# Optimization experiments

Hardware: AMD Instinct MI355X
Metric: run time of the kernel (lower is better)

## Reference

```python
import jax, jax.numpy as jnp
from jax import lax
import numpy as np

N, T, PD, TD, F, E, GB = 2048, 256, 5, 5, 128, 65536, 5


def _lstm_layer(x, Wih, Whh, bih, bhh):
    # x: [B, T, D] -> [B, T, H], torch LSTM gate order (i, f, g, o)
    B = x.shape[0]
    H = Whh.shape[1]
    b = bih + bhh

    def step(carry, xt):
        h, c = carry
        gates = xt @ Wih.T + h @ Whh.T + b
        i, f, g, o = jnp.split(gates, 4, axis=-1)
        c = jax.nn.sigmoid(f) * c + jax.nn.sigmoid(i) * jnp.tanh(g)
        h = jax.nn.sigmoid(o) * jnp.tanh(c)
        return (h, c), h

    h0 = jnp.zeros((B, H), x.dtype)
    _, hs = lax.scan(step, (h0, h0), jnp.swapaxes(x, 0, 1))
    return jnp.swapaxes(hs, 0, 1)


def _attention(x, W1, b1, W2, b2):
    # Fused prefix (cumulative causal) softmax attention.
    # Original loops over t computing softmax(scores[:, :t+1]); here:
    # ctx[t] = cumsum(e * x)[t] / cumsum(e)[t] with a global max shift
    # (softmax is shift-invariant, so this equals the per-prefix softmax).
    s = (jnp.tanh(x @ W1.T + b1) @ W2.T + b2)[..., 0]  # [B, T]
    e = jnp.exp(s - jnp.max(s, axis=1, keepdims=True))  # [B, T]
    num = jnp.cumsum(e[..., None] * x, axis=1)          # [B, T, D]
    den = jnp.cumsum(e, axis=1)[..., None]              # [B, T, 1]
    return jnp.sum(num / den, axis=1)                   # [B, D]


def _gcn(x, W, b, edge_index, edge_weight):
    # PyG GCNConv with normalize=True: add self-loops (w=1), symmetric norm.
    n = x.shape[0]
    loop = jnp.arange(n)
    row = jnp.concatenate([edge_index[0], loop])
    col = jnp.concatenate([edge_index[1], loop])
    w = jnp.concatenate([edge_weight, jnp.ones((n,), edge_weight.dtype)])
    deg = jax.ops.segment_sum(w, col, num_segments=n)
    dinv = jnp.where(deg > 0, deg ** -0.5, 0.0)
    norm = dinv[row] * w * dinv[col]
    h = x @ W.T
    out = jax.ops.segment_sum(norm[:, None] * h[row], col, num_segments=n)
    return out + b


def _forward(price, global_trend, p_weights, t_weights,
             lp_Wih0, lp_Whh0, lp_bih0, lp_bhh0, lp_Wih1, lp_Whh1, lp_bih1, lp_bhh1,
             lt_Wih0, lt_Whh0, lt_bih0, lt_bhh0, lt_Wih1, lt_Whh1, lt_bih1, lt_bhh1,
             ap_W1, ap_b1, ap_W2, ap_b2, at_W1, at_b1, at_W2, at_b2,
             gp1_W, gp1_b, gp2_W, gp2_b, gt1_W, gt1_b, gt2_W, gt2_b,
             mlp_W, mlp_b, p_edge_index, t_edge_index):
    x = _lstm_layer(price, lp_Wih0, lp_Whh0, lp_bih0, lp_bhh0)
    x = _lstm_layer(x, lp_Wih1, lp_Whh1, lp_bih1, lp_bhh1)
    x = _attention(x, ap_W1, ap_b1, ap_W2, ap_b2)            # [N, F]
    g = _lstm_layer(global_trend, lt_Wih0, lt_Whh0, lt_bih0, lt_bhh0)
    g = _lstm_layer(g, lt_Wih1, lt_Whh1, lt_bih1, lt_bhh1)
    g = _attention(g, at_W1, at_b1, at_W2, at_b2)            # [GB, F]
    pg = _gcn(x, gp1_W, gp1_b, p_edge_index, p_weights)
    pg = _gcn(pg, gp2_W, gp2_b, p_edge_index, p_weights)     # [N, F]
    # NOTE: original feeds x (not g) into the trend graph convs.
    tg = _gcn(x, gt1_W, gt1_b, t_edge_index, t_weights)
    tg = _gcn(tg, gt2_W, gt2_b, t_edge_index, t_weights)     # [N, F]
    trend = tg @ g.T                                         # [N, GB]
    feat = jnp.concatenate([pg, trend], axis=1)              # [N, F+GB]
    return jax.nn.sigmoid(feat @ mlp_W.T + mlp_b)            # [N, 1]


def setup_inputs() -> dict:
    key = jax.random.key(0)
    ks = iter(jax.random.split(key, 64))
    nrm = lambda shape, s=0.05: jax.random.normal(next(ks), shape, jnp.float32) * s
    inp = {}
    inp['price'] = jax.random.normal(next(ks), (N, T, PD), jnp.float32)
    inp['global_trend'] = jax.random.normal(next(ks), (GB, T, TD), jnp.float32)
    inp['p_edge_index'] = jax.random.randint(next(ks), (2, E), 0, N)
    inp['p_weights'] = jax.random.uniform(next(ks), (E,), jnp.float32)
    inp['t_edge_index'] = jax.random.randint(next(ks), (2, E), 0, N)
    inp['t_weights'] = jax.random.uniform(next(ks), (E,), jnp.float32)
    for pre, d in (('lp', PD), ('lt', TD)):
        inp[pre + '_Wih0'] = nrm((4 * F, d)); inp[pre + '_Whh0'] = nrm((4 * F, F))
        inp[pre + '_bih0'] = nrm((4 * F,));   inp[pre + '_bhh0'] = nrm((4 * F,))
        inp[pre + '_Wih1'] = nrm((4 * F, F)); inp[pre + '_Whh1'] = nrm((4 * F, F))
        inp[pre + '_bih1'] = nrm((4 * F,));   inp[pre + '_bhh1'] = nrm((4 * F,))
    for pre in ('ap', 'at'):
        inp[pre + '_W1'] = nrm((F, F)); inp[pre + '_b1'] = jnp.zeros((F,), jnp.float32)
        inp[pre + '_W2'] = nrm((1, F)); inp[pre + '_b2'] = jnp.zeros((1,), jnp.float32)
    for pre in ('gp', 'gt'):
        inp[pre + '1_W'] = nrm((16, F)); inp[pre + '1_b'] = jnp.zeros((16,), jnp.float32)
        inp[pre + '2_W'] = nrm((F, 16)); inp[pre + '2_b'] = jnp.zeros((F,), jnp.float32)
    inp['mlp_W'] = nrm((1, F + GB)); inp['mlp_b'] = jnp.zeros((1,), jnp.float32)
    return inp


def reference(price, global_trend, p_edge_index, p_weights, t_edge_index, t_weights,
              lp_Wih0, lp_Whh0, lp_bih0, lp_bhh0, lp_Wih1, lp_Whh1, lp_bih1, lp_bhh1,
              lt_Wih0, lt_Whh0, lt_bih0, lt_bhh0, lt_Wih1, lt_Whh1, lt_bih1, lt_bhh1,
              ap_W1, ap_b1, ap_W2, ap_b2, at_W1, at_b1, at_W2, at_b2,
              gp1_W, gp1_b, gp2_W, gp2_b, gt1_W, gt1_b, gt2_W, gt2_b,
              mlp_W, mlp_b):
    return _forward(price, global_trend, p_weights, t_weights,
                    lp_Wih0, lp_Whh0, lp_bih0, lp_bhh0, lp_Wih1, lp_Whh1, lp_bih1, lp_bhh1,
                    lt_Wih0, lt_Whh0, lt_bih0, lt_bhh0, lt_Wih1, lt_Whh1, lt_bih1, lt_bhh1,
                    ap_W1, ap_b1, ap_W2, ap_b2, at_W1, at_b1, at_W2, at_b2,
                    gp1_W, gp1_b, gp2_W, gp2_b, gt1_W, gt1_b, gt2_W, gt2_b,
                    mlp_W, mlp_b, p_edge_index, t_edge_index)
```

## Files before the change

kernel.cpp:

```cpp
#include <hip/hip_runtime.h>
#include <hip/hip_bf16.h>
#include <cstddef>

#define TT    256
#define NROW  2048
#define GBN   5
#define EDG   65536

using f32x4  = __attribute__((ext_vector_type(4))) float;
using bf16x8 = __attribute__((ext_vector_type(8))) short;

__device__ __forceinline__ void pinv(bf16x8& x) { asm volatile("" : "+v"(x)); }

__device__ __forceinline__ void barrier_lgkm() {
  asm volatile("s_waitcnt lgkmcnt(0)" ::: "memory");
  __builtin_amdgcn_s_barrier();
}

enum : int {
  PK_P0  = 0,
  PK_P1  = 65536,
  PK_PA  = 196608,
  PK_T0  = 212992,
  PK_T1  = 278528,
  PK_TA  = 409600,
  XBUF   = 425984,
  GBUFO  = 688128,
  DINVP  = 688768,
  DINVT  = 690816,
  H16    = 692864,
  PG1    = 725632,
  H128   = 758400,
  PGB    = 1020544,
  TG1    = 1282688,
  TGB    = 1315456,
  WS_END = 1577600
};

enum : int {
  N_P0   = 0,
  N_P1I  = 65536,
  N_P1H  = 131072,
  N_PA   = 196608,
  N_T0   = 212992,
  N_T1I  = 278528,
  N_T1H  = 344064,
  N_TA   = 409600
};

enum : long long {
  C0S_O   = 1577600,
  C1S_O   = 1841792,
  H1IMG_O = 2105984,
  SMST_O  = 2370176,
  NUMS_O  = 2374304,
  ACCOS_O = 2638496,
  H0S_O   = 2902688
};

__device__ __forceinline__ float sigf(float x) { return 1.0f / (1.0f + __expf(-x)); }
__device__ __forceinline__ float tanh_fast(float x) { return 2.0f * sigf(2.0f * x) - 1.0f; }

__global__ void k_pack(const float* __restrict__ Wa, const float* __restrict__ Wb,
                       int K1, int K2, int NT, int KS, ushort* __restrict__ dst) {
  int t = blockIdx.x * blockDim.x + threadIdx.x;
  int total = KS * NT * 2 * 64;
  if (t >= total) return;
  int lane = t & 63;
  int part = (t >> 6) & 1;
  int rest = t >> 7;
  int nt = rest % NT, kk = rest / NT;
  int j = nt * 16 + (lane & 15);
  int kbase = kk * 32 + (lane >> 4) * 8;
  bf16x8 o;
  #pragma unroll
  for (int e = 0; e < 8; ++e) {
    int k = kbase + e;
    float x = (k < K1) ? Wa[(size_t)j * K1 + k] : Wb[(size_t)j * K2 + (k - K1)];
    __hip_bfloat16 hi = __float2bfloat16(x);
    ushort u;
    if (part == 0) {
      u = *(ushort*)&hi;
    } else {
      float lo = x - __bfloat162float(hi);
      __hip_bfloat16 lob = __float2bfloat16(lo);
      u = *(ushort*)&lob;
    }
    o[e] = (short)u;
  }
  ((bf16x8*)dst)[t] = o;
}

__global__ void k_zero(float* __restrict__ p, int n) {
  int i = blockIdx.x * blockDim.x + threadIdx.x;
  if (i < n) p[i] = 0.0f;
}
__global__ void k_fill1(float* __restrict__ p, int n) {
  int i = blockIdx.x * blockDim.x + threadIdx.x;
  if (i < n) p[i] = 1.0f;
}
__global__ void k_deg(const int* __restrict__ col, const float* __restrict__ w,
                      float* __restrict__ deg, int n) {
  int i = blockIdx.x * blockDim.x + threadIdx.x;
  if (i < n) atomicAdd(&deg[col[i]], w[i]);
}
__global__ void k_dinv(float* __restrict__ deg, int n) {
  int i = blockIdx.x * blockDim.x + threadIdx.x;
  if (i < n) deg[i] = rsqrtf(deg[i]);
}

__global__ __launch_bounds__(512, 2) void k_lstm0(
    const float* __restrict__ price, const float* __restrict__ gtrend,
    const float* __restrict__ ws_ro, ushort* __restrict__ h0S, float* __restrict__ c0S,
    const float* __restrict__ Wih0p, const float* __restrict__ bi0p, const float* __restrict__ bh0p,
    const float* __restrict__ Wih0t, const float* __restrict__ bi0t, const float* __restrict__ bh0t,
    int nPrice, int t0, int TCp, int first)
{
  const int tid = threadIdx.x;
  const int w = tid >> 6, l = tid & 63;
  const int lq = l >> 4, lr = l & 15;
  const int rb = lq * 4;
  const int kcol = w * 16 + lr;
  const bool isP = ((int)blockIdx.x) < nPrice;
  const int R = isP ? 16 : GBN;
  const float* seq = isP ? (price + (size_t)blockIdx.x * 16 * (TT * 5)) : gtrend;
  const ushort* S0 = (const ushort*)(ws_ro + (isP ? N_P0 : N_T0));
  const float* Wih0 = isP ? Wih0p : Wih0t;
  const float* bi0 = isP ? bi0p : bi0t;
  const float* bh0 = isP ? bh0p : bh0t;

  __shared__ __align__(16) ushort h0hi[2048], h0lo[2048];
  __shared__ float xs[2][16][5];

  bf16x8 wh[4][4], wl[4][4];
  #pragma unroll
  for (int kk = 0; kk < 4; ++kk)
    #pragma unroll
    for (int g = 0; g < 4; ++g) {
      int blk = (kk * 32 + (w + 8 * g)) * 2;
      wh[kk][g] = ((const bf16x8*)S0)[(blk + 0) * 64 + l];
      wl[kk][g] = ((const bf16x8*)S0)[(blk + 1) * 64 + l];
      pinv(wh[kk][g]); pinv(wl[kk][g]);
    }
  float wih0r[4][5], bg0[4];
  #pragma unroll
  for (int g = 0; g < 4; ++g) {
    int j = kcol + 128 * g;
    bg0[g] = bi0[j] + bh0[j];
    #pragma unroll
    for (int k = 0; k < 5; ++k) wih0r[g][k] = Wih0[j * 5 + k];
  }

  const size_t bstr = (size_t)blockIdx.x * (size_t)TCp * 4096;
  float c0[4] = {0, 0, 0, 0};

  if (first) {
    for (int i = tid; i < 2048; i += 512) { h0hi[i] = 0; h0lo[i] = 0; }
  } else {
    const size_t lb = bstr + (size_t)(TCp - 1) * 4096;
    *(uint2*)&h0hi[4 * tid] = *(const uint2*)&h0S[lb + 4 * tid];
    *(uint2*)&h0lo[4 * tid] = *(const uint2*)&h0S[lb + 2048 + 4 * tid];
    #pragma unroll
    for (int reg = 0; reg < 4; ++reg)
      c0[reg] = c0S[(size_t)blockIdx.x * 2048 + (size_t)(rb + reg) * 128 + kcol];
  }
  const bool stager = (tid >= 64 && tid < 144);
  const int sr = stager ? (tid - 64) / 5 : 0;
  const int sk = stager ? (tid - 64) % 5 : 0;
  if (stager) {
    xs[0][sr][sk] = (sr < R) ? seq[(size_t)sr * (TT * 5) + t0 * 5 + sk] : 0.0f;
  }
  __syncthreads();

  const int kkhi = (kcol >> 3) & 3;
  const int eo = kcol & 7;
  const int b0w = rb + 16 * kkhi;
  const int kkw = kcol >> 5;
  int wro[4];
  #pragma unroll
  for (int reg = 0; reg < 4; ++reg) wro[reg] = kkw * 512 + (b0w + (reg ^ lq)) * 8 + eo;
  const int rdo = (l ^ ((l >> 2) & 3)) * 8;

  for (int tl = 0; tl < TCp; ++tl) {
    const int xb = tl & 1;
    float xld = 0.0f;
    if (stager && tl + 1 < TCp)
      xld = (sr < R) ? seq[(size_t)sr * (TT * 5) + (size_t)(t0 + tl + 1) * 5 + sk] : 0.0f;

    f32x4 acc[4];
    #pragma unroll
    for (int g = 0; g < 4; ++g) acc[g] = (f32x4){bg0[g], bg0[g], bg0[g], bg0[g]};
    #pragma unroll
    for (int k = 0; k < 5; ++k) {
      float xv[4];
      #pragma unroll
      for (int reg = 0; reg < 4; ++reg) xv[reg] = xs[xb][rb + reg][k];
      #pragma unroll
      for (int g = 0; g < 4; ++g)
        #pragma unroll
        for (int reg = 0; reg < 4; ++reg)
          acc[g][reg] = fmaf(xv[reg], wih0r[g][k], acc[g][reg]);
    }
    #pragma unroll
    for (int kk = 0; kk < 4; ++kk) {
      bf16x8 ah = *(const bf16x8*)&h0hi[kk * 512 + rdo];
      bf16x8 al = *(const bf16x8*)&h0lo[kk * 512 + rdo];
      #pragma unroll
      for (int g = 0; g < 4; ++g) {
        acc[g] = __builtin_amdgcn_mfma_f32_16x16x32_bf16(ah, wh[kk][g], acc[g], 0, 0, 0);
        acc[g] = __builtin_amdgcn_mfma_f32_16x16x32_bf16(al, wh[kk][g], acc[g], 0, 0, 0);
        acc[g] = __builtin_amdgcn_mfma_f32_16x16x32_bf16(ah, wl[kk][g], acc[g], 0, 0, 0);
      }
    }
    barrier_lgkm();
    #pragma unroll
    for (int reg = 0; reg < 4; ++reg) {
      float gi = acc[0][reg], gf = acc[1][reg], gg = acc[2][reg], go = acc[3][reg];
      float c = sigf(gf) * c0[reg] + sigf(gi) * tanh_fast(gg);
      c0[reg] = c;
      float h = sigf(go) * tanh_fast(c);
      __hip_bfloat16 hb = __float2bfloat16(h);
      float lo = h - __bfloat162float(hb);
      __hip_bfloat16 lb = __float2bfloat16(lo);
      h0hi[wro[reg]] = *(ushort*)&hb;
      h0lo[wro[reg]] = *(ushort*)&lb;
    }
    if (stager && tl + 1 < TCp) xs[xb ^ 1][sr][sk] = xld;
    barrier_lgkm();
    *(uint2*)&h0S[bstr + (size_t)tl * 4096 + 4 * tid] = *(const uint2*)&h0hi[4 * tid];
    *(uint2*)&h0S[bstr + (size_t)tl * 4096 + 2048 + 4 * tid] = *(const uint2*)&h0lo[4 * tid];
  }

  #pragma unroll
  for (int reg = 0; reg < 4; ++reg)
    c0S[(size_t)blockIdx.x * 2048 + (size_t)(rb + reg) * 128 + kcol] = c0[reg];
}

__global__ __launch_bounds__(512, 2) void k_pre1(
    const ushort* __restrict__ h0S, const float* __restrict__ ws_ro,
    float* __restrict__ pre1,
    const float* __restrict__ bi1p, const float* __restrict__ bh1p,
    const float* __restrict__ bi1t, const float* __restrict__ bh1t,
    int nPrice, int TCp, int nsub)
{
  const int b = blockIdx.x / nsub, sub = blockIdx.x % nsub;
  const int tid = threadIdx.x;
  const int w = tid >> 6, l = tid & 63;
  const int lr = l & 15;
  const int kcol = w * 16 + lr;
  const bool isP = b < nPrice;
  const ushort* S1I = (const ushort*)(ws_ro + (isP ? N_P1I : N_T1I));
  const float* bi1 = isP ? bi1p : bi1t;
  const float* bh1 = isP ? bh1p : bh1t;
  float bg1[4];
  #pragma unroll
  for (int g = 0; g < 4; ++g) bg1[g] = bi1[kcol + 128 * g] + bh1[kcol + 128 * g];
  const int rdo = (l ^ ((l >> 2) & 3)) * 8;
  const size_t bstr = (size_t)b * (size_t)TCp * 4096;
  const int t0 = sub * 4;

  f32x4 acc[4][4];
  #pragma unroll
  for (int ts = 0; ts < 4; ++ts)
    #pragma unroll
    for (int g = 0; g < 4; ++g) acc[ts][g] = (f32x4){bg1[g], bg1[g], bg1[g], bg1[g]};

  #pragma unroll
  for (int kk = 0; kk < 4; ++kk) {
    bf16x8 bh_[4], bl_[4];
    #pragma unroll
    for (int g = 0; g < 4; ++g) {
      int blk = (kk * 32 + (w + 8 * g)) * 2;
      bh_[g] = ((const bf16x8*)S1I)[(blk + 0) * 64 + l];
      bl_[g] = ((const bf16x8*)S1I)[(blk + 1) * 64 + l];
    }
    #pragma unroll
    for (int ts = 0; ts < 4; ++ts) {
      const size_t tb = bstr + (size_t)(t0 + ts) * 4096 + kk * 512 + rdo;
      bf16x8 ah = *(const bf16x8*)&h0S[tb];
      bf16x8 al = *(const bf16x8*)&h0S[tb + 2048];
      #pragma unroll
      for (int g = 0; g < 4; ++g) {
        acc[ts][g] = __builtin_amdgcn_mfma_f32_16x16x32_bf16(ah, bh_[g], acc[ts][g], 0, 0, 0);
        acc[ts][g] = __builtin_amdgcn_mfma_f32_16x16x32_bf16(al, bh_[g], acc[ts][g], 0, 0, 0);
        acc[ts][g] = __builtin_amdgcn_mfma_f32_16x16x32_bf16(ah, bl_[g], acc[ts][g], 0, 0, 0);
      }
    }
  }
  #pragma unroll
  for (int ts = 0; ts < 4; ++ts)
    #pragma unroll
    for (int g = 0; g < 4; ++g)
      *(f32x4*)&pre1[((size_t)b * TCp + (t0 + ts)) * 8192 + (size_t)tid * 16 + g * 4] = acc[ts][g];
}

__global__ __launch_bounds__(512, 2) void k_lstm1(
    const float* __restrict__ pre1, const float* __restrict__ ws_ro,
    float* __restrict__ xout, float* __restrict__ gout,
    float* __restrict__ c1S, ushort* __restrict__ h1imgS, float* __restrict__ smS,
    float* __restrict__ numS, float* __restrict__ accOS,
    const float* __restrict__ apB1, const float* __restrict__ apW2, const float* __restrict__ apB2,
    const float* __restrict__ atB1, const float* __restrict__ atW2, const float* __restrict__ atB2,
    int nPrice, int t0, int TCp, int first)
{
  const int tid = threadIdx.x;
  const int w = tid >> 6, l = tid & 63;
  const int lq = l >> 4, lr = l & 15;
  const int rb = lq * 4;
  const int kcol = w * 16 + lr;
  const bool isP = ((int)blockIdx.x) < nPrice;
  const int R = isP ? 16 : GBN;
  const ushort* S1H = (const ushort*)(ws_ro + (isP ? N_P1H : N_T1H));
  const ushort* SA  = (const ushort*)(ws_ro + (isP ? N_PA : N_TA));
  const float* b1ap = isP ? apB1 : atB1;
  const float* w2p  = isP ? apW2 : atW2;
  const float  b2v  = isP ? apB2[0] : atB2[0];

  __shared__ __align__(16) ushort h1hi[2048], h1lo[2048];
  __shared__ float sbuf[8][16];

  bf16x8 hh[4][4], hl[4][4];
  #pragma unroll
  for (int kk = 0; kk < 4; ++kk)
    #pragma unroll
    for (int g = 0; g < 4; ++g) {
      int blk = (kk * 32 + (w + 8 * g)) * 2;
      hh[kk][g] = ((const bf16x8*)S1H)[(blk + 0) * 64 + l];
      hl[kk][g] = ((const bf16x8*)S1H)[(blk + 1) * 64 + l];
      pinv(hh[kk][g]); pinv(hl[kk][g]);
    }
  bf16x8 wa[4], wal[4];
  #pragma unroll
  for (int kk = 0; kk < 4; ++kk) {
    wa[kk]  = ((const bf16x8*)SA)[((kk * 8 + w) * 2 + 0) * 64 + l];
    wal[kk] = ((const bf16x8*)SA)[((kk * 8 + w) * 2 + 1) * 64 + l];
    pinv(wa[kk]); pinv(wal[kk]);
  }
  const float w2r = w2p[kcol], b1ar = b1ap[kcol];

  float c1[4] = {0, 0, 0, 0}, h1r[4] = {0, 0, 0, 0};
  float num[4] = {0, 0, 0, 0}, accO[4] = {0, 0, 0, 0};
  float m_run[4], den_r[4];

  if (first) {
    for (int i = tid; i < 2048; i += 512) { h1hi[i] = 0; h1lo[i] = 0; }
    #pragma unroll
    for (int reg = 0; reg < 4; ++reg) { m_run[reg] = -1e30f; den_r[reg] = 0.0f; }
  } else {
    const size_t ib = (size_t)blockIdx.x * 4096;
    *(uint2*)&h1hi[4 * tid] = *(const uint2*)&h1imgS[ib + 4 * tid];
    *(uint2*)&h1lo[4 * tid] = *(const uint2*)&h1imgS[ib + 2048 + 4 * tid];
    const size_t sb = (size_t)blockIdx.x * 2048;
    #pragma unroll
    for (int reg = 0; reg < 4; ++reg) {
      size_t o = sb + (size_t)(rb + reg) * 128 + kcol;
      c1[reg] = c1S[o];
      num[reg] = numS[o];
      accO[reg] = accOS[o];
      m_run[reg] = smS[(size_t)blockIdx.x * 32 + (size_t)(rb + reg) * 2];
      den_r[reg] = smS[(size_t)blockIdx.x * 32 + (size_t)(rb + reg) * 2 + 1];
    }
  }
  __syncthreads();

  const int kkhi = (kcol >> 3) & 3;
  const int eo = kcol & 7;
  const int b0w = rb + 16 * kkhi;
  const int kkw = kcol >> 5;
  int wro[4];
  #pragma unroll
  for (int reg = 0; reg < 4; ++reg) wro[reg] = kkw * 512 + (b0w + (reg ^ lq)) * 8 + eo;
  const int rdo = (l ^ ((l >> 2) & 3)) * 8;

  const float* pbase = pre1 + (size_t)blockIdx.x * TCp * 8192 + (size_t)tid * 16;

  f32x4 pnext[4];
  #pragma unroll
  for (int g = 0; g < 4; ++g) pnext[g] = *(const f32x4*)&pbase[g * 4];

  for (int tl = 0; tl < TCp; ++tl) {
    f32x4 acc[4];
    #pragma unroll
    for (int g = 0; g < 4; ++g) acc[g] = pnext[g];
    if (tl + 1 < TCp) {
      #pragma unroll
      for (int g = 0; g < 4; ++g)
        pnext[g] = *(const f32x4*)&pbase[(size_t)(tl + 1) * 8192 + g * 4];
    }

    #pragma unroll
    for (int kk = 0; kk < 4; ++kk) {
      bf16x8 ah = *(const bf16x8*)&h1hi[kk * 512 + rdo];
      bf16x8 al = *(const bf16x8*)&h1lo[kk * 512 + rdo];
      #pragma unroll
      for (int g = 0; g < 4; ++g) {
        acc[g] = __builtin_amdgcn_mfma_f32_16x16x32_bf16(ah, hh[kk][g], acc[g], 0, 0, 0);
        acc[g] = __builtin_amdgcn_mfma_f32_16x16x32_bf16(al, hh[kk][g], acc[g], 0, 0, 0);
        acc[g] = __builtin_amdgcn_mfma_f32_16x16x32_bf16(ah, hl[kk][g], acc[g], 0, 0, 0);
      }
    }
    barrier_lgkm();
    #pragma unroll
    for (int reg = 0; reg < 4; ++reg) {
      float gi = acc[0][reg], gf = acc[1][reg], gg = acc[2][reg], go = acc[3][reg];
      float c = sigf(gf) * c1[reg] + sigf(gi) * tanh_fast(gg);
      c1[reg] = c;
      float h = sigf(go) * tanh_fast(c);
      h1r[reg] = h;
      __hip_bfloat16 hb = __float2bfloat16(h);
      float lo = h - __bfloat162float(hb);
      __hip_bfloat16 lb = __float2bfloat16(lo);
      h1hi[wro[reg]] = *(ushort*)&hb;
      h1lo[wro[reg]] = *(ushort*)&lb;
    }
    barrier_lgkm();

    f32x4 aa = (f32x4){b1ar, b1ar, b1ar, b1ar};
    #pragma unroll
    for (int kk = 0; kk < 4; ++kk) {
      bf16x8 ah = *(const bf16x8*)&h1hi[kk * 512 + rdo];
      bf16x8 al = *(const bf16x8*)&h1lo[kk * 512 + rdo];
      aa = __builtin_amdgcn_mfma_f32_16x16x32_bf16(ah, wa[kk], aa, 0, 0, 0);
      aa = __builtin_amdgcn_mfma_f32_16x16x32_bf16(al, wa[kk], aa, 0, 0, 0);
      aa = __builtin_amdgcn_mfma_f32_16x16x32_bf16(ah, wal[kk], aa, 0, 0, 0);
    }
    float p[4];
    #pragma unroll
    for (int reg = 0; reg < 4; ++reg) p[reg] = tanh_fast(aa[reg]) * w2r;
    #pragma unroll
    for (int m = 1; m < 16; m <<= 1) {
      #pragma unroll
      for (int reg = 0; reg < 4; ++reg) p[reg] += __shfl_xor(p[reg], m);
    }
    if (lr == 0) {
      #pragma unroll
      for (int reg = 0; reg < 4; ++reg) sbuf[w][rb + reg] = p[reg];
    }
    barrier_lgkm();
    #pragma unroll
    for (int reg = 0; reg < 4; ++reg) {
      float s = b2v;
      #pragma unroll
      for (int ww = 0; ww < 8; ++ww) s += sbuf[ww][rb + reg];
      float m0 = m_run[reg];
      float nm = fmaxf(m0, s);
      float e = __expf(s - nm), sc = __expf(m0 - nm);
      float d = den_r[reg] * sc + e;
      m_run[reg] = nm; den_r[reg] = d;
      num[reg] = num[reg] * sc + e * h1r[reg];
      accO[reg] = fmaf(num[reg], 1.0f / d, accO[reg]);
    }
  }

  {
    const size_t ib = (size_t)blockIdx.x * 4096;
    *(uint2*)&h1imgS[ib + 4 * tid] = *(const uint2*)&h1hi[4 * tid];
    *(uint2*)&h1imgS[ib + 2048 + 4 * tid] = *(const uint2*)&h1lo[4 * tid];
    const size_t sb = (size_t)blockIdx.x * 2048;
    #pragma unroll
    for (int reg = 0; reg < 4; ++reg) {
      size_t o = sb + (size_t)(rb + reg) * 128 + kcol;
      c1S[o] = c1[reg];
      numS[o] = num[reg];
      accOS[o] = accO[reg];
    }
    if (w == 0 && lr == 0) {
      #pragma unroll
      for (int reg = 0; reg < 4; ++reg) {
        smS[(size_t)blockIdx.x * 32 + (size_t)(rb + reg) * 2] = m_run[reg];
        smS[(size_t)blockIdx.x * 32 + (size_t)(rb + reg) * 2 + 1] = den_r[reg];
      }
    }
  }

  float* dstx = isP ? (xout + (size_t)blockIdx.x * 16 * 128) : gout;
  #pragma unroll
  for (int reg = 0; reg < 4; ++reg) {
    int r = rb + reg;
    if (r < R) dstx[(size_t)r * 128 + kcol] = accO[reg];
  }
}

__global__ void k_lin(const float* __restrict__ x, const float* __restrict__ W,
                      float* __restrict__ h, int M, int K, int n) {
  int i = blockIdx.x * blockDim.x + threadIdx.x;
  if (i >= n) return;
  int r = i / M, m = i % M;
  const float* xr = x + (size_t)r * K;
  const float* wm = W + (size_t)m * K;
  float a = 0.f;
  for (int k = 0; k < K; ++k) a = fmaf(xr[k], wm[k], a);
  h[i] = a;
}

__global__ void k_scatter(const int* __restrict__ rowi, const int* __restrict__ coli,
                          const float* __restrict__ w, const float* __restrict__ dinv,
                          const float* __restrict__ h, float* __restrict__ outp,
                          int M, long long n) {
  long long i = (long long)blockIdx.x * blockDim.x + threadIdx.x;
  if (i >= n) return;
  int e = (int)(i / M), f = (int)(i % M);
  int rs = rowi[e], cd = coli[e];
  float nrm = dinv[rs] * w[e] * dinv[cd];
  atomicAdd(&outp[(size_t)cd * M + f], nrm * h[(size_t)rs * M + f]);
}

__global__ void k_gcn_fin(float* __restrict__ io, const float* __restrict__ h,
                          const float* __restrict__ dinv, const float* __restrict__ b,
                          int M, int n) {
  int i = blockIdx.x * blockDim.x + threadIdx.x;
  if (i >= n) return;
  int v = i / M, f = i % M;
  float dv = dinv[v];
  io[i] += dv * dv * h[i] + b[f];
}

__global__ __launch_bounds__(256) void k_final(const float* __restrict__ pg, const float* __restrict__ tg,
                                               const float* __restrict__ g, const float* __restrict__ mw,
                                               const float* __restrict__ mb, float* __restrict__ outp) {
  int wv = threadIdx.x >> 6, ln = threadIdx.x & 63;
  int r = blockIdx.x * 4 + wv;
  const float* pr = pg + (size_t)r * 128;
  const float* tr = tg + (size_t)r * 128;
  float pa = pr[ln] * mw[ln] + pr[ln + 64] * mw[ln + 64];
  float t0 = tr[ln], t1 = tr[ln + 64];
  float s[GBN];
  #pragma unroll
  for (int gb = 0; gb < GBN; ++gb)
    s[gb] = g[gb * 128 + ln] * t0 + g[gb * 128 + 64 + ln] * t1;
  #pragma unroll
  for (int o = 32; o > 0; o >>= 1) {
    pa += __shfl_down(pa, o);
    #pragma unroll
    for (int gb = 0; gb < GBN; ++gb) s[gb] += __shfl_down(s[gb], o);
  }
  if (ln == 0) {
    float lg = pa + mb[0];
    #pragma unroll
    for (int gb = 0; gb < GBN; ++gb) lg = fmaf(s[gb], mw[128 + gb], lg);
    outp[r] = 1.0f / (1.0f + __expf(-lg));
  }
}

static inline int gdiv(long long n) { return (int)((n + 255) / 256); }

extern "C" void kernel_launch(void* const* d_in, const int* in_sizes, int n_in,
                              void* d_out, int out_size, void* d_ws, size_t ws_size,
                              hipStream_t stream) {
  const float* price  = (const float*)d_in[0];
  const float* gtrend = (const float*)d_in[1];
  const int*   p_ei   = (const int*)d_in[2];
  const float* p_w    = (const float*)d_in[3];
  const int*   t_ei   = (const int*)d_in[4];
  const float* t_w    = (const float*)d_in[5];
  const float* lpWih0 = (const float*)d_in[6];
  const float* lpWhh0 = (const float*)d_in[7];
  const float* lpBih0 = (const float*)d_in[8];
  const float* lpBhh0 = (const float*)d_in[9];
  const float* lpWih1 = (const float*)d_in[10];
  const float* lpWhh1 = (const float*)d_in[11];
  const float* lpBih1 = (const float*)d_in[12];
  const float* lpBhh1 = (const float*)d_in[13];
  const float* ltWih0 = (const float*)d_in[14];
  const float* ltWhh0 = (const float*)d_in[15];
  const float* ltBih0 = (const float*)d_in[16];
  const float* ltBhh0 = (const float*)d_in[17];
  const float* ltWih1 = (const float*)d_in[18];
  const float* ltWhh1 = (const float*)d_in[19];
  const float* ltBih1 = (const float*)d_in[20];
  const float* ltBhh1 = (const float*)d_in[21];
  const float* apW1 = (const float*)d_in[22];
  const float* apB1 = (const float*)d_in[23];
  const float* apW2 = (const float*)d_in[24];
  const float* apB2 = (const float*)d_in[25];
  const float* atW1 = (const float*)d_in[26];
  const float* atB1 = (const float*)d_in[27];
  const float* atW2 = (const float*)d_in[28];
  const float* atB2 = (const float*)d_in[29];
  const float* gp1W = (const float*)d_in[30];
  const float* gp1b = (const float*)d_in[31];
  const float* gp2W = (const float*)d_in[32];
  const float* gp2b = (const float*)d_in[33];
  const float* gt1W = (const float*)d_in[34];
  const float* gt1b = (const float*)d_in[35];
  const float* gt2W = (const float*)d_in[36];
  const float* gt2b = (const float*)d_in[37];
  const float* mlpW = (const float*)d_in[38];
  const float* mlpb = (const float*)d_in[39];

  float* ws = (float*)d_ws;
  float* outp = (float*)d_out;
  if (ws_size < (size_t)WS_END * sizeof(float)) return;

  int TC = 0;
  for (int cand = 32; cand >= 8; cand >>= 1) {
    unsigned long long need = ((unsigned long long)H0S_O + 129ULL * cand * (2048ULL + 8192ULL)) * 4ULL;
    if ((unsigned long long)ws_size >= need) { TC = cand; break; }
  }

  if (TC > 0) {
    k_pack<<<gdiv(16384), 256, 0, stream>>>(lpWhh0, lpWhh0, 128, 128, 32, 4, (ushort*)(ws + N_P0));
    k_pack<<<gdiv(16384), 256, 0, stream>>>(lpWih1, lpWih1, 128, 128, 32, 4, (ushort*)(ws + N_P1I));
    k_pack<<<gdiv(16384), 256, 0, stream>>>(lpWhh1, lpWhh1, 128, 128, 32, 4, (ushort*)(ws + N_P1H));
    k_pack<<<gdiv(4096),  256, 0, stream>>>(apW1,   apW1,   128, 128,  8, 4, (ushort*)(ws + N_PA));
    k_pack<<<gdiv(16384), 256, 0, stream>>>(ltWhh0, ltWhh0, 128, 128, 32, 4, (ushort*)(ws + N_T0));
    k_pack<<<gdiv(16384), 256, 0, stream>>>(ltWih1, ltWih1, 128, 128, 32, 4, (ushort*)(ws + N_T1I));
    k_pack<<<gdiv(16384), 256, 0, stream>>>(ltWhh1, ltWhh1, 128, 128, 32, 4, (ushort*)(ws + N_T1H));
    k_pack<<<gdiv(4096),  256, 0, stream>>>(atW1,   atW1,   128, 128,  8, 4, (ushort*)(ws + N_TA));
  } else {
    return;
  }

  k_fill1<<<gdiv(NROW), 256, 0, stream>>>(ws + DINVP, NROW);
  k_deg<<<gdiv(EDG), 256, 0, stream>>>(p_ei + EDG, p_w, ws + DINVP, EDG);
  k_dinv<<<gdiv(NROW), 256, 0, stream>>>(ws + DINVP, NROW);
  k_fill1<<<gdiv(NROW), 256, 0, stream>>>(ws + DINVT, NROW);
  k_deg<<<gdiv(EDG), 256, 0, stream>>>(t_ei + EDG, t_w, ws + DINVT, EDG);
  k_dinv<<<gdiv(NROW), 256, 0, stream>>>(ws + DINVT, NROW);

  {
    const int CH = TT / TC;
    const int nsub = TC / 4;
    ushort* h0S = (ushort*)(ws + H0S_O);
    float*  pre1 = ws + H0S_O + (long long)129 * TC * 2048;
    for (int c = 0; c < CH; ++c) {
      k_lstm0<<<129, 512, 0, stream>>>(price, gtrend, ws, h0S, ws + C0S_O,
                                       lpWih0, lpBih0, lpBhh0,
                                       ltWih0, ltBih0, ltBhh0,
                                       128, c * TC, TC, c == 0 ? 1 : 0);
      k_pre1<<<129 * nsub, 512, 0, stream>>>(h0S, ws, pre1,
                                             lpBih1, lpBhh1, ltBih1, ltBhh1,
                                             128, TC, nsub);
      k_lstm1<<<129, 512, 0, stream>>>(pre1, ws,
                                       ws + XBUF, ws + GBUFO,
                                       ws + C1S_O, (ushort*)(ws + H1IMG_O), ws + SMST_O,
                                       ws + NUMS_O, ws + ACCOS_O,
                                       apB1, apW2, apB2,
                                       atB1, atW2, atB2,
                                       128, c * TC, TC, c == 0 ? 1 : 0);
    }
  }

  k_lin<<<gdiv(NROW * 16), 256, 0, stream>>>(ws + XBUF, gp1W, ws + H16, 16, 128, NROW * 16);
  k_zero<<<gdiv(NROW * 16), 256, 0, stream>>>(ws + PG1, NROW * 16);
  k_scatter<<<gdiv((long long)EDG * 16), 256, 0, stream>>>(p_ei, p_ei + EDG, p_w, ws + DINVP,
                                                           ws + H16, ws + PG1, 16, (long long)EDG * 16);
  k_gcn_fin<<<gdiv(NROW * 16), 256, 0, stream>>>(ws + PG1, ws + H16, ws + DINVP, gp1b, 16, NROW * 16);
  k_lin<<<gdiv(NROW * 128), 256, 0, stream>>>(ws + PG1, gp2W, ws + H128, 128, 16, NROW * 128);
  k_zero<<<gdiv(NROW * 128), 256, 0, stream>>>(ws + PGB, NROW * 128);
  k_scatter<<<gdiv((long long)EDG * 128), 256, 0, stream>>>(p_ei, p_ei + EDG, p_w, ws + DINVP,
                                                            ws + H128, ws + PGB, 128, (long long)EDG * 128);
  k_gcn_fin<<<gdiv(NROW * 128), 256, 0, stream>>>(ws + PGB, ws + H128, ws + DINVP, gp2b, 128, NROW * 128);

  k_lin<<<gdiv(NROW * 16), 256, 0, stream>>>(ws + XBUF, gt1W, ws + H16, 16, 128, NROW * 16);
  k_zero<<<gdiv(NROW * 16), 256, 0, stream>>>(ws + TG1, NROW * 16);
  k_scatter<<<gdiv((long long)EDG * 16), 256, 0, stream>>>(t_ei, t_ei + EDG, t_w, ws + DINVT,
                                                           ws + H16, ws + TG1, 16, (long long)EDG * 16);
  k_gcn_fin<<<gdiv(NROW * 16), 256, 0, stream>>>(ws + TG1, ws + H16, ws + DINVT, gt1b, 16, NROW * 16);
  k_lin<<<gdiv(NROW * 128), 256, 0, stream>>>(ws + TG1, gt2W, ws + H128, 128, 16, NROW * 128);
  k_zero<<<gdiv(NROW * 128), 256, 0, stream>>>(ws + TGB, NROW * 128);
  k_scatter<<<gdiv((long long)EDG * 128), 256, 0, stream>>>(t_ei, t_ei + EDG, t_w, ws + DINVT,
                                                            ws + H128, ws + TGB, 128, (long long)EDG * 128);
  k_gcn_fin<<<gdiv(NROW * 128), 256, 0, stream>>>(ws + TGB, ws + H128, ws + DINVT, gt2b, 128, NROW * 128);

  k_final<<<512, 256, 0, stream>>>(ws + PGB, ws + TGB, ws + GBUFO, mlpW, mlpb, outp);
}
```

Measured before the change: 2.552 ms.

## Double-buffer LSTM hidden state, fold input projection into lstm1, defer attention reduction

The hidden-state tiles in shared memory for both LSTM layers are now double-buffered, so one of the two barriers per timestep is dropped. In lstm0 the global h0S store is moved to the next iteration to overlap with compute. The separate k_pre1 launch is removed and its input-projection GEMM runs inside k_lstm1 before the recurrence. In lstm1 the attention softmax reduction is lagged by one step to avoid a second barrier, and the chunk size search now starts at 64 to cut launch count. The fused projection costs only 129 blocks of parallelism, where k_pre1 spread it over many more blocks, and it uses more shared memory.

```diff
diff --git a/kernel.cpp b/kernel.cpp
--- a/kernel.cpp
+++ b/kernel.cpp
@@ -18,12 +18,6 @@
 }
 
 enum : int {
-  PK_P0  = 0,
-  PK_P1  = 65536,
-  PK_PA  = 196608,
-  PK_T0  = 212992,
-  PK_T1  = 278528,
-  PK_TA  = 409600,
   XBUF   = 425984,
   GBUFO  = 688128,
   DINVP  = 688768,
@@ -129,7 +123,7 @@
   const float* bi0 = isP ? bi0p : bi0t;
   const float* bh0 = isP ? bh0p : bh0t;
 
-  __shared__ __align__(16) ushort h0hi[2048], h0lo[2048];
+  __shared__ __align__(16) ushort h0hi[2][2048], h0lo[2][2048];
   __shared__ float xs[2][16][5];
 
   bf16x8 wh[4][4], wl[4][4];
@@ -155,11 +149,11 @@
   float c0[4] = {0, 0, 0, 0};
 
   if (first) {
-    for (int i = tid; i < 2048; i += 512) { h0hi[i] = 0; h0lo[i] = 0; }
+    for (int i = tid; i < 2048; i += 512) { h0hi[0][i] = 0; h0lo[0][i] = 0; }
   } else {
     const size_t lb = bstr + (size_t)(TCp - 1) * 4096;
-    *(uint2*)&h0hi[4 * tid] = *(const uint2*)&h0S[lb + 4 * tid];
-    *(uint2*)&h0lo[4 * tid] = *(const uint2*)&h0S[lb + 2048 + 4 * tid];
+    *(uint2*)&h0hi[0][4 * tid] = *(const uint2*)&h0S[lb + 4 * tid];
+    *(uint2*)&h0lo[0][4 * tid] = *(const uint2*)&h0S[lb + 2048 + 4 * tid];
     #pragma unroll
     for (int reg = 0; reg < 4; ++reg)
       c0[reg] = c0S[(size_t)blockIdx.x * 2048 + (size_t)(rb + reg) * 128 + kcol];
@@ -181,11 +175,17 @@
   for (int reg = 0; reg < 4; ++reg) wro[reg] = kkw * 512 + (b0w + (reg ^ lq)) * 8 + eo;
   const int rdo = (l ^ ((l >> 2) & 3)) * 8;
 
+  int cur = 0;
   for (int tl = 0; tl < TCp; ++tl) {
     const int xb = tl & 1;
+    const int nxt = cur ^ 1;
     float xld = 0.0f;
     if (stager && tl + 1 < TCp)
       xld = (sr < R) ? seq[(size_t)sr * (TT * 5) + (size_t)(t0 + tl + 1) * 5 + sk] : 0.0f;
+    if (tl > 0) {
+      *(uint2*)&h0S[bstr + (size_t)(tl - 1) * 4096 + 4 * tid] = *(const uint2*)&h0hi[cur][4 * tid];
+      *(uint2*)&h0S[bstr + (size_t)(tl - 1) * 4096 + 2048 + 4 * tid] = *(const uint2*)&h0lo[cur][4 * tid];
+    }
 
     f32x4 acc[4];
     #pragma unroll
@@ -203,8 +203,8 @@
     }
     #pragma unroll
     for (int kk = 0; kk < 4; ++kk) {
-      bf16x8 ah = *(const bf16x8*)&h0hi[kk * 512 + rdo];
-      bf16x8 al = *(const bf16x8*)&h0lo[kk * 512 + rdo];
+      bf16x8 ah = *(const bf16x8*)&h0hi[cur][kk * 512 + rdo];
+      bf16x8 al = *(const bf16x8*)&h0lo[cur][kk * 512 + rdo];
       #pragma unroll
       for (int g = 0; g < 4; ++g) {
         acc[g] = __builtin_amdgcn_mfma_f32_16x16x32_bf16(ah, wh[kk][g], acc[g], 0, 0, 0);
@@ -212,7 +212,6 @@
         acc[g] = __builtin_amdgcn_mfma_f32_16x16x32_bf16(ah, wl[kk][g], acc[g], 0, 0, 0);
       }
     }
-    barrier_lgkm();
     #pragma unroll
     for (int reg = 0; reg < 4; ++reg) {
       float gi = acc[0][reg], gf = acc[1][reg], gg = acc[2][reg], go = acc[3][reg];
@@ -222,84 +221,29 @@
       __hip_bfloat16 hb = __float2bfloat16(h);
       float lo = h - __bfloat162float(hb);
       __hip_bfloat16 lb = __float2bfloat16(lo);
-      h0hi[wro[reg]] = *(ushort*)&hb;
-      h0lo[wro[reg]] = *(ushort*)&lb;
+      h0hi[nxt][wro[reg]] = *(ushort*)&hb;
+      h0lo[nxt][wro[reg]] = *(ushort*)&lb;
     }
     if (stager && tl + 1 < TCp) xs[xb ^ 1][sr][sk] = xld;
     barrier_lgkm();
-    *(uint2*)&h0S[bstr + (size_t)tl * 4096 + 4 * tid] = *(const uint2*)&h0hi[4 * tid];
-    *(uint2*)&h0S[bstr + (size_t)tl * 4096 + 2048 + 4 * tid] = *(const uint2*)&h0lo[4 * tid];
-  }
+    cur = nxt;
+  }
+  *(uint2*)&h0S[bstr + (size_t)(TCp - 1) * 4096 + 4 * tid] = *(const uint2*)&h0hi[cur][4 * tid];
+  *(uint2*)&h0S[bstr + (size_t)(TCp - 1) * 4096 + 2048 + 4 * tid] = *(const uint2*)&h0lo[cur][4 * tid];
 
   #pragma unroll
   for (int reg = 0; reg < 4; ++reg)
     c0S[(size_t)blockIdx.x * 2048 + (size_t)(rb + reg) * 128 + kcol] = c0[reg];
 }
 
-__global__ __launch_bounds__(512, 2) void k_pre1(
-    const ushort* __restrict__ h0S, const float* __restrict__ ws_ro,
-    float* __restrict__ pre1,
-    const float* __restrict__ bi1p, const float* __restrict__ bh1p,
-    const float* __restrict__ bi1t, const float* __restrict__ bh1t,
-    int nPrice, int TCp, int nsub)
-{
-  const int b = blockIdx.x / nsub, sub = blockIdx.x % nsub;
-  const int tid = threadIdx.x;
-  const int w = tid >> 6, l = tid & 63;
-  const int lr = l & 15;
-  const int kcol = w * 16 + lr;
-  const bool isP = b < nPrice;
-  const ushort* S1I = (const ushort*)(ws_ro + (isP ? N_P1I : N_T1I));
-  const float* bi1 = isP ? bi1p : bi1t;
-  const float* bh1 = isP ? bh1p : bh1t;
-  float bg1[4];
-  #pragma unroll
-  for (int g = 0; g < 4; ++g) bg1[g] = bi1[kcol + 128 * g] + bh1[kcol + 128 * g];
-  const int rdo = (l ^ ((l >> 2) & 3)) * 8;
-  const size_t bstr = (size_t)b * (size_t)TCp * 4096;
-  const int t0 = sub * 4;
-
-  f32x4 acc[4][4];
-  #pragma unroll
-  for (int ts = 0; ts < 4; ++ts)
-    #pragma unroll
-    for (int g = 0; g < 4; ++g) acc[ts][g] = (f32x4){bg1[g], bg1[g], bg1[g], bg1[g]};
-
-  #pragma unroll
-  for (int kk = 0; kk < 4; ++kk) {
-    bf16x8 bh_[4], bl_[4];
-    #pragma unroll
-    for (int g = 0; g < 4; ++g) {
-      int blk = (kk * 32 + (w + 8 * g)) * 2;
-      bh_[g] = ((const bf16x8*)S1I)[(blk + 0) * 64 + l];
-      bl_[g] = ((const bf16x8*)S1I)[(blk + 1) * 64 + l];
-    }
-    #pragma unroll
-    for (int ts = 0; ts < 4; ++ts) {
-      const size_t tb = bstr + (size_t)(t0 + ts) * 4096 + kk * 512 + rdo;
-      bf16x8 ah = *(const bf16x8*)&h0S[tb];
-      bf16x8 al = *(const bf16x8*)&h0S[tb + 2048];
-      #pragma unroll
-      for (int g = 0; g < 4; ++g) {
-        acc[ts][g] = __builtin_amdgcn_mfma_f32_16x16x32_bf16(ah, bh_[g], acc[ts][g], 0, 0, 0);
-        acc[ts][g] = __builtin_amdgcn_mfma_f32_16x16x32_bf16(al, bh_[g], acc[ts][g], 0, 0, 0);
-        acc[ts][g] = __builtin_amdgcn_mfma_f32_16x16x32_bf16(ah, bl_[g], acc[ts][g], 0, 0, 0);
-      }
-    }
-  }
-  #pragma unroll
-  for (int ts = 0; ts < 4; ++ts)
-    #pragma unroll
-    for (int g = 0; g < 4; ++g)
-      *(f32x4*)&pre1[((size_t)b * TCp + (t0 + ts)) * 8192 + (size_t)tid * 16 + g * 4] = acc[ts][g];
-}
-
 __global__ __launch_bounds__(512, 2) void k_lstm1(
-    const float* __restrict__ pre1, const float* __restrict__ ws_ro,
+    const ushort* __restrict__ h0S, float* __restrict__ pre1, const float* __restrict__ ws_ro,
     float* __restrict__ xout, float* __restrict__ gout,
     float* __restrict__ c1S, ushort* __restrict__ h1imgS, float* __restrict__ smS,
     float* __restrict__ numS, float* __restrict__ accOS,
+    const float* __restrict__ bi1p, const float* __restrict__ bh1p,
     const float* __restrict__ apB1, const float* __restrict__ apW2, const float* __restrict__ apB2,
+    const float* __restrict__ bi1t, const float* __restrict__ bh1t,
     const float* __restrict__ atB1, const float* __restrict__ atW2, const float* __restrict__ atB2,
     int nPrice, int t0, int TCp, int first)
 {
@@ -310,14 +254,61 @@
   const int kcol = w * 16 + lr;
   const bool isP = ((int)blockIdx.x) < nPrice;
   const int R = isP ? 16 : GBN;
+  const ushort* S1I = (const ushort*)(ws_ro + (isP ? N_P1I : N_T1I));
   const ushort* S1H = (const ushort*)(ws_ro + (isP ? N_P1H : N_T1H));
   const ushort* SA  = (const ushort*)(ws_ro + (isP ? N_PA : N_TA));
+  const float* bi1 = isP ? bi1p : bi1t;
+  const float* bh1 = isP ? bh1p : bh1t;
   const float* b1ap = isP ? apB1 : atB1;
   const float* w2p  = isP ? apW2 : atW2;
   const float  b2v  = isP ? apB2[0] : atB2[0];
 
-  __shared__ __align__(16) ushort h1hi[2048], h1lo[2048];
-  __shared__ float sbuf[8][16];
+  __shared__ __align__(16) ushort h1hi[2][2048], h1lo[2][2048];
+  __shared__ float sbuf[2][8][16];
+
+  const int rdo = (l ^ ((l >> 2) & 3)) * 8;
+  const size_t bstr = (size_t)blockIdx.x * (size_t)TCp * 4096;
+  float* pblk = pre1 + (size_t)blockIdx.x * TCp * 8192;
+
+  float bg1[4];
+  #pragma unroll
+  for (int g = 0; g < 4; ++g) bg1[g] = bi1[kcol + 128 * g] + bh1[kcol + 128 * g];
+
+  for (int g0 = 0; g0 < TCp; g0 += 2) {
+    f32x4 pacc[2][4];
+    #pragma unroll
+    for (int ts = 0; ts < 2; ++ts)
+      #pragma unroll
+      for (int g = 0; g < 4; ++g) pacc[ts][g] = (f32x4){bg1[g], bg1[g], bg1[g], bg1[g]};
+    #pragma unroll
+    for (int kk = 0; kk < 4; ++kk) {
+      bf16x8 bh_[4], bl_[4];
+      #pragma unroll
+      for (int g = 0; g < 4; ++g) {
+        int blk = (kk * 32 + (w + 8 * g)) * 2;
+        bh_[g] = ((const bf16x8*)S1I)[(blk + 0) * 64 + l];
+        bl_[g] = ((const bf16x8*)S1I)[(blk + 1) * 64 + l];
+      }
+      #pragma unroll
+      for (int ts = 0; ts < 2; ++ts) {
+        const size_t tb = bstr + (size_t)(g0 + ts) * 4096 + kk * 512 + rdo;
+        bf16x8 ah = *(const bf16x8*)&h0S[tb];
+        bf16x8 al = *(const bf16x8*)&h0S[tb + 2048];
+        #pragma unroll
+        for (int g = 0; g < 4; ++g) {
+          pacc[ts][g] = __builtin_amdgcn_mfma_f32_16x16x32_bf16(ah, bh_[g], pacc[ts][g], 0, 0, 0);
+          pacc[ts][g] = __builtin_amdgcn_mfma_f32_16x16x32_bf16(al, bh_[g], pacc[ts][g], 0, 0, 0);
+          pacc[ts][g] = __builtin_amdgcn_mfma_f32_16x16x32_bf16(ah, bl_[g], pacc[ts][g], 0, 0, 0);
+        }
+      }
+    }
+    #pragma unroll
+    for (int ts = 0; ts < 2; ++ts)
+      #pragma unroll
+      for (int g = 0; g < 4; ++g)
+        *(f32x4*)&pblk[(size_t)(g0 + ts) * 8192 + (size_t)tid * 16 + g * 4] = pacc[ts][g];
+  }
+  asm volatile("s_waitcnt vmcnt(0)" ::: "memory");
 
   bf16x8 hh[4][4], hl[4][4];
   #pragma unroll
@@ -338,18 +329,18 @@
   }
   const float w2r = w2p[kcol], b1ar = b1ap[kcol];
 
-  float c1[4] = {0, 0, 0, 0}, h1r[4] = {0, 0, 0, 0};
+  float c1[4] = {0, 0, 0, 0}, h1r[4] = {0, 0, 0, 0}, h1r_prev[4];
   float num[4] = {0, 0, 0, 0}, accO[4] = {0, 0, 0, 0};
   float m_run[4], den_r[4];
 
   if (first) {
-    for (int i = tid; i < 2048; i += 512) { h1hi[i] = 0; h1lo[i] = 0; }
+    for (int i = tid; i < 2048; i += 512) { h1hi[0][i] = 0; h1lo[0][i] = 0; }
     #pragma unroll
     for (int reg = 0; reg < 4; ++reg) { m_run[reg] = -1e30f; den_r[reg] = 0.0f; }
   } else {
     const size_t ib = (size_t)blockIdx.x * 4096;
-    *(uint2*)&h1hi[4 * tid] = *(const uint2*)&h1imgS[ib + 4 * tid];
-    *(uint2*)&h1lo[4 * tid] = *(const uint2*)&h1imgS[ib + 2048 + 4 * tid];
+    *(uint2*)&h1hi[0][4 * tid] = *(const uint2*)&h1imgS[ib + 4 * tid];
+    *(uint2*)&h1lo[0][4 * tid] = *(const uint2*)&h1imgS[ib + 2048 + 4 * tid];
     const size_t sb = (size_t)blockIdx.x * 2048;
     #pragma unroll
     for (int reg = 0; reg < 4; ++reg) {
@@ -370,15 +361,16 @@
   int wro[4];
   #pragma unroll
   for (int reg = 0; reg < 4; ++reg) wro[reg] = kkw * 512 + (b0w + (reg ^ lq)) * 8 + eo;
-  const int rdo = (l ^ ((l >> 2) & 3)) * 8;
-
-  const float* pbase = pre1 + (size_t)blockIdx.x * TCp * 8192 + (size_t)tid * 16;
+
+  const float* pbase = pblk + (size_t)tid * 16;
 
   f32x4 pnext[4];
   #pragma unroll
   for (int g = 0; g < 4; ++g) pnext[g] = *(const f32x4*)&pbase[g * 4];
 
+  int cur = 0;
   for (int tl = 0; tl < TCp; ++tl) {
+    const int nxt = cur ^ 1;
     f32x4 acc[4];
     #pragma unroll
     for (int g = 0; g < 4; ++g) acc[g] = pnext[g];
@@ -390,8 +382,8 @@
 
     #pragma unroll
     for (int kk = 0; kk < 4; ++kk) {
-      bf16x8 ah = *(const bf16x8*)&h1hi[kk * 512 + rdo];
-      bf16x8 al = *(const bf16x8*)&h1lo[kk * 512 + rdo];
+      bf16x8 ah = *(const bf16x8*)&h1hi[cur][kk * 512 + rdo];
+      bf16x8 al = *(const bf16x8*)&h1lo[cur][kk * 512 + rdo];
       #pragma unroll
       for (int g = 0; g < 4; ++g) {
         acc[g] = __builtin_amdgcn_mfma_f32_16x16x32_bf16(ah, hh[kk][g], acc[g], 0, 0, 0);
@@ -399,9 +391,9 @@
         acc[g] = __builtin_amdgcn_mfma_f32_16x16x32_bf16(ah, hl[kk][g], acc[g], 0, 0, 0);
       }
     }
-    barrier_lgkm();
     #pragma unroll
     for (int reg = 0; reg < 4; ++reg) {
+      h1r_prev[reg] = h1r[reg];
       float gi = acc[0][reg], gf = acc[1][reg], gg = acc[2][reg], go = acc[3][reg];
       float c = sigf(gf) * c1[reg] + sigf(gi) * tanh_fast(gg);
       c1[reg] = c;
@@ -410,16 +402,33 @@
       __hip_bfloat16 hb = __float2bfloat16(h);
       float lo = h - __bfloat162float(hb);
       __hip_bfloat16 lb = __float2bfloat16(lo);
-      h1hi[wro[reg]] = *(ushort*)&hb;
-      h1lo[wro[reg]] = *(ushort*)&lb;
+      h1hi[nxt][wro[reg]] = *(ushort*)&hb;
+      h1lo[nxt][wro[reg]] = *(ushort*)&lb;
     }
     barrier_lgkm();
 
+    if (tl > 0) {
+      const int pb = (tl - 1) & 1;
+      #pragma unroll
+      for (int reg = 0; reg < 4; ++reg) {
+        float s = b2v;
+        #pragma unroll
+        for (int ww = 0; ww < 8; ++ww) s += sbuf[pb][ww][rb + reg];
+        float m0 = m_run[reg];
+        float nm = fmaxf(m0, s);
+        float e = __expf(s - nm), sc = __expf(m0 - nm);
+        float d = den_r[reg] * sc + e;
+        m_run[reg] = nm; den_r[reg] = d;
+        num[reg] = num[reg] * sc + e * h1r_prev[reg];
+        accO[reg] = fmaf(num[reg], 1.0f / d, accO[reg]);
+      }
+    }
+
     f32x4 aa = (f32x4){b1ar, b1ar, b1ar, b1ar};
     #pragma unroll
     for (int kk = 0; kk < 4; ++kk) {
-      bf16x8 ah = *(const bf16x8*)&h1hi[kk * 512 + rdo];
-      bf16x8 al = *(const bf16x8*)&h1lo[kk * 512 + rdo];
+      bf16x8 ah = *(const bf16x8*)&h1hi[nxt][kk * 512 + rdo];
+      bf16x8 al = *(const bf16x8*)&h1lo[nxt][kk * 512 + rdo];
       aa = __builtin_amdgcn_mfma_f32_16x16x32_bf16(ah, wa[kk], aa, 0, 0, 0);
       aa = __builtin_amdgcn_mfma_f32_16x16x32_bf16(al, wa[kk], aa, 0, 0, 0);
       aa = __builtin_amdgcn_mfma_f32_16x16x32_bf16(ah, wal[kk], aa, 0, 0, 0);
@@ -434,14 +443,18 @@
     }
     if (lr == 0) {
       #pragma unroll
-      for (int reg = 0; reg < 4; ++reg) sbuf[w][rb + reg] = p[reg];
-    }
-    barrier_lgkm();
+      for (int reg = 0; reg < 4; ++reg) sbuf[tl & 1][w][rb + reg] = p[reg];
+    }
+    cur = nxt;
+  }
+  barrier_lgkm();
+  {
+    const int pb = (TCp - 1) & 1;
     #pragma unroll
     for (int reg = 0; reg < 4; ++reg) {
       float s = b2v;
       #pragma unroll
-      for (int ww = 0; ww < 8; ++ww) s += sbuf[ww][rb + reg];
+      for (int ww = 0; ww < 8; ++ww) s += sbuf[pb][ww][rb + reg];
       float m0 = m_run[reg];
       float nm = fmaxf(m0, s);
       float e = __expf(s - nm), sc = __expf(m0 - nm);
@@ -454,8 +467,8 @@
 
   {
     const size_t ib = (size_t)blockIdx.x * 4096;
-    *(uint2*)&h1imgS[ib + 4 * tid] = *(const uint2*)&h1hi[4 * tid];
-    *(uint2*)&h1imgS[ib + 2048 + 4 * tid] = *(const uint2*)&h1lo[4 * tid];
+    *(uint2*)&h1imgS[ib + 4 * tid] = *(const uint2*)&h1hi[cur][4 * tid];
+    *(uint2*)&h1imgS[ib + 2048 + 4 * tid] = *(const uint2*)&h1lo[cur][4 * tid];
     const size_t sb = (size_t)blockIdx.x * 2048;
     #pragma unroll
     for (int reg = 0; reg < 4; ++reg) {
@@ -593,23 +606,20 @@
   if (ws_size < (size_t)WS_END * sizeof(float)) return;
 
   int TC = 0;
-  for (int cand = 32; cand >= 8; cand >>= 1) {
+  for (int cand = 64; cand >= 8; cand >>= 1) {
     unsigned long long need = ((unsigned long long)H0S_O + 129ULL * cand * (2048ULL + 8192ULL)) * 4ULL;
     if ((unsigned long long)ws_size >= need) { TC = cand; break; }
   }
-
-  if (TC > 0) {
-    k_pack<<<gdiv(16384), 256, 0, stream>>>(lpWhh0, lpWhh0, 128, 128, 32, 4, (ushort*)(ws + N_P0));
-    k_pack<<<gdiv(16384), 256, 0, stream>>>(lpWih1, lpWih1, 128, 128, 32, 4, (ushort*)(ws + N_P1I));
-    k_pack<<<gdiv(16384), 256, 0, stream>>>(lpWhh1, lpWhh1, 128, 128, 32, 4, (ushort*)(ws + N_P1H));
-    k_pack<<<gdiv(4096),  256, 0, stream>>>(apW1,   apW1,   128, 128,  8, 4, (ushort*)(ws + N_PA));
-    k_pack<<<gdiv(16384), 256, 0, stream>>>(ltWhh0, ltWhh0, 128, 128, 32, 4, (ushort*)(ws + N_T0));
-    k_pack<<<gdiv(16384), 256, 0, stream>>>(ltWih1, ltWih1, 128, 128, 32, 4, (ushort*)(ws + N_T1I));
-    k_pack<<<gdiv(16384), 256, 0, stream>>>(ltWhh1, ltWhh1, 128, 128, 32, 4, (ushort*)(ws + N_T1H));
-    k_pack<<<gdiv(4096),  256, 0, stream>>>(atW1,   atW1,   128, 128,  8, 4, (ushort*)(ws + N_TA));
-  } else {
-    return;
-  }
+  if (TC == 0) return;
+
+  k_pack<<<gdiv(16384), 256, 0, stream>>>(lpWhh0, lpWhh0, 128, 128, 32, 4, (ushort*)(ws + N_P0));
+  k_pack<<<gdiv(16384), 256, 0, stream>>>(lpWih1, lpWih1, 128, 128, 32, 4, (ushort*)(ws + N_P1I));
+  k_pack<<<gdiv(16384), 256, 0, stream>>>(lpWhh1, lpWhh1, 128, 128, 32, 4, (ushort*)(ws + N_P1H));
+  k_pack<<<gdiv(4096),  256, 0, stream>>>(apW1,   apW1,   128, 128,  8, 4, (ushort*)(ws + N_PA));
+  k_pack<<<gdiv(16384), 256, 0, stream>>>(ltWhh0, ltWhh0, 128, 128, 32, 4, (ushort*)(ws + N_T0));
+  k_pack<<<gdiv(16384), 256, 0, stream>>>(ltWih1, ltWih1, 128, 128, 32, 4, (ushort*)(ws + N_T1I));
+  k_pack<<<gdiv(16384), 256, 0, stream>>>(ltWhh1, ltWhh1, 128, 128, 32, 4, (ushort*)(ws + N_T1H));
+  k_pack<<<gdiv(4096),  256, 0, stream>>>(atW1,   atW1,   128, 128,  8, 4, (ushort*)(ws + N_TA));
 
   k_fill1<<<gdiv(NROW), 256, 0, stream>>>(ws + DINVP, NROW);
   k_deg<<<gdiv(EDG), 256, 0, stream>>>(p_ei + EDG, p_w, ws + DINVP, EDG);
@@ -620,7 +630,6 @@
 
   {
     const int CH = TT / TC;
-    const int nsub = TC / 4;
     ushort* h0S = (ushort*)(ws + H0S_O);
     float*  pre1 = ws + H0S_O + (long long)129 * TC * 2048;
     for (int c = 0; c < CH; ++c) {
@@ -628,15 +637,12 @@
                                        lpWih0, lpBih0, lpBhh0,
                                        ltWih0, ltBih0, ltBhh0,
                                        128, c * TC, TC, c == 0 ? 1 : 0);
-      k_pre1<<<129 * nsub, 512, 0, stream>>>(h0S, ws, pre1,
-                                             lpBih1, lpBhh1, ltBih1, ltBhh1,
-                                             128, TC, nsub);
-      k_lstm1<<<129, 512, 0, stream>>>(pre1, ws,
+      k_lstm1<<<129, 512, 0, stream>>>(h0S, pre1, ws,
                                        ws + XBUF, ws + GBUFO,
                                        ws + C1S_O, (ushort*)(ws + H1IMG_O), ws + SMST_O,
                                        ws + NUMS_O, ws + ACCOS_O,
-                                       apB1, apW2, apB2,
-                                       atB1, atW2, atB2,
+                                       lpBih1, lpBhh1, apB1, apW2, apB2,
+                                       ltBih1, ltBhh1, atB1, atW2, atB2,
                                        128, c * TC, TC, c == 0 ? 1 : 0);
     }
   }
```

Measured after the change: 2.718 ms. 1.06x slower.
